# Optimization experiments

Hardware: AMD Instinct MI355X
Metric: run time of the kernel (lower is better)

The kernel has to match this reference:

```python
import jax, jax.numpy as jnp
import numpy as np

DIM = 192; HEADS = 6; WS = 7; RES = 56; SHIFT = 3
HEAD_DIM = DIM // HEADS
SCALE = HEAD_DIM ** -0.5
N = WS * WS
EPS = 1e-5

def _rel_pos_index():
    coords = np.stack(np.meshgrid(np.arange(WS), np.arange(WS), indexing='ij')).reshape(2, -1)
    rel = coords[:, :, None] - coords[:, None, :]  # [2,N,N]
    rel = rel.transpose(1, 2, 0)
    rel[:, :, 0] += WS - 1
    rel[:, :, 1] += WS - 1
    rel[:, :, 0] *= 2 * WS - 1
    return rel.sum(-1)  # [N,N]

def _attn_mask():
    img = np.zeros((RES, RES), dtype=np.float32)
    slices = (slice(0, -WS), slice(-WS, -SHIFT), slice(-SHIFT, None))
    cnt = 0
    for h in slices:
        for w in slices:
            img[h, w] = cnt; cnt += 1
    mw = img.reshape(RES // WS, WS, RES // WS, WS).transpose(0, 2, 1, 3).reshape(-1, N)  # [nW,N]
    diff = mw[:, None, :] - mw[:, :, None]
    return np.where(diff != 0, -100.0, 0.0).astype(np.float32)  # [nW,N,N]

REL_IDX = jnp.asarray(_rel_pos_index())
ATTN_MASK = jnp.asarray(_attn_mask())

def _ln(x, g, b):
    mu = x.mean(-1, keepdims=True)
    var = ((x - mu) ** 2).mean(-1, keepdims=True)
    return (x - mu) * jax.lax.rsqrt(var + EPS) * g + b

def setup_inputs() -> dict:
    key = jax.random.key(0)
    ks = jax.random.split(key, 8)
    d = {
        'x': jax.random.normal(ks[0], (32, RES * RES, DIM), jnp.float32),
        'norm1_g': jnp.ones((DIM,), jnp.float32), 'norm1_b': jnp.zeros((DIM,), jnp.float32),
        'qkv_w': jax.random.normal(ks[1], (DIM, 3 * DIM), jnp.float32) * 0.02,
        'qkv_b': jnp.zeros((3 * DIM,), jnp.float32),
        'proj_w': jax.random.normal(ks[2], (DIM, DIM), jnp.float32) * 0.02,
        'proj_b': jnp.zeros((DIM,), jnp.float32),
        'bias_table': jax.random.normal(ks[3], ((2 * WS - 1) ** 2, HEADS), jnp.float32) * 0.02,
        'norm2_g': jnp.ones((DIM,), jnp.float32), 'norm2_b': jnp.zeros((DIM,), jnp.float32),
        'fc1_w': jax.random.normal(ks[4], (DIM, 4 * DIM), jnp.float32) * 0.02,
        'fc1_b': jnp.zeros((4 * DIM,), jnp.float32),
        'fc2_w': jax.random.normal(ks[5], (4 * DIM, DIM), jnp.float32) * 0.02,
        'fc2_b': jnp.zeros((DIM,), jnp.float32),
    }
    return d

def reference(x, norm1_g, norm1_b, qkv_w, qkv_b, proj_w, proj_b, bias_table,
              norm2_g, norm2_b, fc1_w, fc1_b, fc2_w, fc2_b):
    B, L, C = x.shape
    H = W = RES
    shortcut = x
    h = _ln(x, norm1_g, norm1_b).reshape(B, H, W, C)
    # cyclic shift
    h = jnp.roll(h, (-SHIFT, -SHIFT), axis=(1, 2))
    # window partition -> [B*nW, N, C]
    nH = H // WS
    h = h.reshape(B, nH, WS, nH, WS, C).transpose(0, 1, 3, 2, 4, 5).reshape(-1, N, C)
    BW = h.shape[0]
    # windowed MHSA
    qkv = (h @ qkv_w + qkv_b).reshape(BW, N, 3, HEADS, HEAD_DIM)
    q, k, v = qkv[:, :, 0], qkv[:, :, 1], qkv[:, :, 2]  # [BW,N,h,hd]
    attn = jnp.einsum('bnhd,bmhd->bhnm', q, k) * SCALE  # [BW,h,N,N]
    bias = bias_table[REL_IDX.reshape(-1)].reshape(N, N, HEADS).transpose(2, 0, 1)
    attn = attn + bias[None]
    nW = ATTN_MASK.shape[0]
    attn = attn.reshape(BW // nW, nW, HEADS, N, N) + ATTN_MASK[None, :, None]
    attn = jax.nn.softmax(attn.reshape(BW, HEADS, N, N), axis=-1)
    h = jnp.einsum('bhnm,bmhd->bnhd', attn, v).reshape(BW, N, C)
    h = h @ proj_w + proj_b
    # window reverse
    h = h.reshape(B, nH, nH, WS, WS, C).transpose(0, 1, 3, 2, 4, 5).reshape(B, H, W, C)
    h = jnp.roll(h, (SHIFT, SHIFT), axis=(1, 2)).reshape(B, L, C)
    x = shortcut + h
    # MLP
    m = _ln(x, norm2_g, norm2_b)
    m = jax.nn.gelu(m @ fc1_w + fc1_b, approximate=False) @ fc2_w + fc2_b
    return x + m
```

## Files before the change

### kernel.cpp

```cpp
#include <hip/hip_runtime.h>
#include <hip/hip_bf16.h>
#include <math.h>

typedef __attribute__((ext_vector_type(8))) short bh8;
typedef __attribute__((ext_vector_type(4))) float fx4;

__device__ __forceinline__ fx4 mfma_bf16(bh8 a, bh8 b, fx4 c) {
    return __builtin_amdgcn_mfma_f32_16x16x32_bf16(a, b, c, 0, 0, 0);
}

__device__ __forceinline__ void gload16(const __hip_bfloat16* g, __hip_bfloat16* l) {
    __builtin_amdgcn_global_load_lds(
        (const __attribute__((address_space(1))) void*)g,
        (__attribute__((address_space(3))) void*)l,
        16, 0, 0);
}

__device__ __forceinline__ float fast_erf(float u) {
    float au = fabsf(u);
    float t  = __builtin_amdgcn_rcpf(1.0f + 0.3275911f * au);
    float p  = ((((1.061405429f * t - 1.453152027f) * t + 1.421413741f) * t
                 - 0.284496736f) * t + 0.254829592f) * t;
    float e  = __expf(-u * u);
    return copysignf(1.0f - p * e, u);
}

__global__ __launch_bounds__(256)
void convw_k(const float* __restrict__ W, __hip_bfloat16* __restrict__ Wt, int K, int Nn)
{
    int idx = blockIdx.x * 256 + threadIdx.x;
    if (idx < K * Nn) {
        int k = idx / Nn, n = idx - k * Nn;
        Wt[(size_t)n * K + k] = __float2bfloat16(W[idx]);
    }
}

__global__ __launch_bounds__(256)
void ln1_gather_k(const float* __restrict__ x, const float* __restrict__ g,
                  const float* __restrict__ bia, __hip_bfloat16* __restrict__ xw)
{
    const int wave = threadIdx.x >> 6, lane = threadIdx.x & 63;
    const int t = blockIdx.x * 4 + wave;
    const int w = t / 49, n = t - w * 49;
    const int b = w >> 6, wrem = w & 63, wi = wrem >> 3, wj = wrem & 7;
    const int i = n / 7, j = n - i * 7;
    int sr = wi * 7 + i + 3; if (sr >= 56) sr -= 56;
    int sc = wj * 7 + j + 3; if (sc >= 56) sc -= 56;
    const float* xp = x + ((size_t)b * 3136 + sr * 56 + sc) * 192;
    float v0 = xp[lane], v1 = xp[lane + 64], v2 = xp[lane + 128];
    float s = v0 + v1 + v2;
    float q = v0 * v0 + v1 * v1 + v2 * v2;
    for (int off = 32; off > 0; off >>= 1) {
        s += __shfl_down(s, off, 64);
        q += __shfl_down(q, off, 64);
    }
    s = __shfl(s, 0, 64); q = __shfl(q, 0, 64);
    float mean = s * (1.0f / 192.0f);
    float var  = q * (1.0f / 192.0f) - mean * mean;
    float rstd = rsqrtf(var + 1e-5f);
    __hip_bfloat16* op = xw + (size_t)t * 192;
    op[lane]       = __float2bfloat16((v0 - mean) * rstd * g[lane]       + bia[lane]);
    op[lane + 64]  = __float2bfloat16((v1 - mean) * rstd * g[lane + 64]  + bia[lane + 64]);
    op[lane + 128] = __float2bfloat16((v2 - mean) * rstd * g[lane + 128] + bia[lane + 128]);
}

template<int MODE, int K, int NOUT>
__global__ __launch_bounds__(256)
void gemm2_k(const __hip_bfloat16* __restrict__ A,
             const __hip_bfloat16* __restrict__ Bt,
             const float* __restrict__ bias,
             const float* __restrict__ resid,
             void* __restrict__ outv)
{
    __shared__ __align__(16) __hip_bfloat16 As[128 * 32];
    __shared__ __align__(16) __hip_bfloat16 Bs[64 * 32];
    const int tid  = threadIdx.x;
    const int lane = tid & 63, wave = tid >> 6;
    const int quad = lane >> 4, l15 = lane & 15;
    const int m0 = blockIdx.x * 128, n0 = blockIdx.y * 64;

    const int arow = lane >> 2, acol = (lane & 3) * 8;
    const __hip_bfloat16* Ag0 = A  + (size_t)(m0 + wave * 32 + arow)      * K + acol;
    const __hip_bfloat16* Ag1 = A  + (size_t)(m0 + wave * 32 + 16 + arow) * K + acol;
    const __hip_bfloat16* Bg  = Bt + (size_t)(n0 + wave * 16 + arow)      * K + acol;
    __hip_bfloat16* Al0 = &As[(wave * 32)      * 32];
    __hip_bfloat16* Al1 = &As[(wave * 32 + 16) * 32];
    __hip_bfloat16* Bl  = &Bs[(wave * 16)      * 32];

    fx4 acc[2][4];
#pragma unroll
    for (int mi = 0; mi < 2; mi++)
#pragma unroll
        for (int ni = 0; ni < 4; ni++) acc[mi][ni] = {0.f, 0.f, 0.f, 0.f};

    for (int k0 = 0; k0 < K; k0 += 32) {
        gload16(Ag0 + k0, Al0);
        gload16(Ag1 + k0, Al1);
        gload16(Bg  + k0, Bl);
        __syncthreads();
        bh8 a0 = *(const bh8*)&As[(wave * 32 + l15)      * 32 + quad * 8];
        bh8 a1 = *(const bh8*)&As[(wave * 32 + 16 + l15) * 32 + quad * 8];
        bh8 b0 = *(const bh8*)&Bs[(0 * 16 + l15) * 32 + quad * 8];
        bh8 b1 = *(const bh8*)&Bs[(1 * 16 + l15) * 32 + quad * 8];
        bh8 b2 = *(const bh8*)&Bs[(2 * 16 + l15) * 32 + quad * 8];
        bh8 b3 = *(const bh8*)&Bs[(3 * 16 + l15) * 32 + quad * 8];
        acc[0][0] = mfma_bf16(a0, b0, acc[0][0]);
        acc[0][1] = mfma_bf16(a0, b1, acc[0][1]);
        acc[0][2] = mfma_bf16(a0, b2, acc[0][2]);
        acc[0][3] = mfma_bf16(a0, b3, acc[0][3]);
        acc[1][0] = mfma_bf16(a1, b0, acc[1][0]);
        acc[1][1] = mfma_bf16(a1, b1, acc[1][1]);
        acc[1][2] = mfma_bf16(a1, b2, acc[1][2]);
        acc[1][3] = mfma_bf16(a1, b3, acc[1][3]);
        __syncthreads();
    }

#pragma unroll
    for (int mi = 0; mi < 2; mi++)
#pragma unroll
    for (int ni = 0; ni < 4; ni++) {
        const int n = n0 + ni * 16 + l15;
        const float bn = bias[n];
#pragma unroll
        for (int r = 0; r < 4; r++) {
            const int m = m0 + wave * 32 + mi * 16 + quad * 4 + r;
            float v = acc[mi][ni][r] + bn;
            if (MODE == 0) {
                if (n < 192) v *= 0.17677669529663687f;
                ((__hip_bfloat16*)outv)[(size_t)m * NOUT + n] = __float2bfloat16(v);
            } else if (MODE == 2) {
                v = 0.5f * v * (1.0f + erff(v * 0.70710678118654752f));
                ((__hip_bfloat16*)outv)[(size_t)m * NOUT + n] = __float2bfloat16(v);
            } else {
                ((float*)outv)[(size_t)m * NOUT + n] = v + resid[(size_t)m * NOUT + n];
            }
        }
    }
}

__global__ __launch_bounds__(256)
void mlp_k(const __hip_bfloat16* __restrict__ A,
           const __hip_bfloat16* __restrict__ W1t,
           const __hip_bfloat16* __restrict__ W2t,
           const float* __restrict__ b1,
           const float* __restrict__ b2,
           float* __restrict__ out)
{
    __shared__ __align__(16) __hip_bfloat16 W1s[2][6][32][32];
    __shared__ __align__(16) __hip_bfloat16 W2s[2][192][32];
    __shared__ __align__(16) __hip_bfloat16 Hs[64][40];

    const int tid  = threadIdx.x;
    const int lane = tid & 63, wave = tid >> 6;
    const int quad = lane >> 4, l15 = lane & 15;
    const int m0 = blockIdx.x * 64;
    const int arow = lane >> 2, acol = (lane & 3) * 8;

    bh8 xr[6];
    const __hip_bfloat16* xg = A + (size_t)(m0 + wave * 16 + l15) * 192 + quad * 8;
#pragma unroll
    for (int kc = 0; kc < 6; kc++) xr[kc] = *(const bh8*)(xg + kc * 32);

    auto stage = [&](int bf, int c) {
#pragma unroll
        for (int i = 0; i < 3; i++) {
            const int g = wave * 3 + i;
            const int kc = g >> 1, half = g & 1;
            gload16(W1t + (size_t)(c * 32 + half * 16 + arow) * 192 + kc * 32 + acol,
                    &W1s[bf][kc][half * 16][0]);
            gload16(W2t + (size_t)(g * 16 + arow) * 768 + c * 32 + acol,
                    &W2s[bf][g * 16][0]);
        }
    };

    fx4 acc2[12];
#pragma unroll
    for (int nt = 0; nt < 12; nt++) acc2[nt] = {0.f, 0.f, 0.f, 0.f};

    stage(0, 0);
    __syncthreads();

    int cur = 0;
    for (int c = 0; c < 24; c++) {
        if (c < 23) stage(cur ^ 1, c + 1);

        float b1v0 = b1[c * 32 + l15];
        float b1v1 = b1[c * 32 + 16 + l15];

        fx4 acc1[2];
        acc1[0] = {0.f, 0.f, 0.f, 0.f};
        acc1[1] = {0.f, 0.f, 0.f, 0.f};
#pragma unroll
        for (int kc = 0; kc < 6; kc++) {
#pragma unroll
            for (int ni = 0; ni < 2; ni++) {
                bh8 b = *(const bh8*)&W1s[cur][kc][ni * 16 + l15][quad * 8];
                acc1[ni] = mfma_bf16(xr[kc], b, acc1[ni]);
            }
        }

#pragma unroll
        for (int ni = 0; ni < 2; ni++) {
            const float bb = ni ? b1v1 : b1v0;
#pragma unroll
            for (int r = 0; r < 4; r++) {
                float v = acc1[ni][r] + bb;
                float h = 0.5f * v * (1.0f + fast_erf(v * 0.70710678118654752f));
                Hs[wave * 16 + quad * 4 + r][ni * 16 + l15] = __float2bfloat16(h);
            }
        }
        asm volatile("s_waitcnt lgkmcnt(0)" ::: "memory");
        __builtin_amdgcn_sched_barrier(0);

        bh8 ap = *(const bh8*)&Hs[wave * 16 + l15][quad * 8];
#pragma unroll
        for (int nt = 0; nt < 12; nt++) {
            bh8 b = *(const bh8*)&W2s[cur][nt * 16 + l15][quad * 8];
            acc2[nt] = mfma_bf16(ap, b, acc2[nt]);
        }

        __syncthreads();
        cur ^= 1;
    }

#pragma unroll
    for (int nt = 0; nt < 12; nt++) {
        const int n = nt * 16 + l15;
        const float bn = b2[n];
#pragma unroll
        for (int r = 0; r < 4; r++) {
            const int m = m0 + wave * 16 + quad * 4 + r;
            out[(size_t)m * 192 + n] += acc2[nt][r] + bn;
        }
    }
}

__global__ __launch_bounds__(256)
void projln_k(const __hip_bfloat16* __restrict__ A,
              const __hip_bfloat16* __restrict__ Bt,
              const float* __restrict__ pb,
              const float* __restrict__ xresid,
              const float* __restrict__ g2,
              const float* __restrict__ b2,
              float* __restrict__ x1out,
              __hip_bfloat16* __restrict__ y2out)
{
    __shared__ __align__(16) __hip_bfloat16 As[64 * 32];
    __shared__ __align__(16) __hip_bfloat16 Bs[192 * 32];
    const int tid  = threadIdx.x;
    const int lane = tid & 63, wave = tid >> 6;
    const int quad = lane >> 4, l15 = lane & 15;
    const int m0 = blockIdx.x * 64;

    const int arow = lane >> 2, acol = (lane & 3) * 8;
    const __hip_bfloat16* Ag = A + (size_t)(m0 + wave * 16 + arow) * 192 + acol;
    __hip_bfloat16* Al = &As[(wave * 16) * 32];
    const __hip_bfloat16* Bg0 = Bt + (size_t)((wave + 0) * 16 + arow) * 192 + acol;
    const __hip_bfloat16* Bg1 = Bt + (size_t)((wave + 4) * 16 + arow) * 192 + acol;
    const __hip_bfloat16* Bg2 = Bt + (size_t)((wave + 8) * 16 + arow) * 192 + acol;
    __hip_bfloat16* Bl0 = &Bs[((wave + 0) * 16) * 32];
    __hip_bfloat16* Bl1 = &Bs[((wave + 4) * 16) * 32];
    __hip_bfloat16* Bl2 = &Bs[((wave + 8) * 16) * 32];

    fx4 acc[12];
#pragma unroll
    for (int ct = 0; ct < 12; ct++) acc[ct] = {0.f, 0.f, 0.f, 0.f};

    for (int k0 = 0; k0 < 192; k0 += 32) {
        gload16(Ag  + k0, Al);
        gload16(Bg0 + k0, Bl0);
        gload16(Bg1 + k0, Bl1);
        gload16(Bg2 + k0, Bl2);
        __syncthreads();
        bh8 a = *(const bh8*)&As[(wave * 16 + l15) * 32 + quad * 8];
#pragma unroll
        for (int ct = 0; ct < 12; ct++) {
            bh8 b = *(const bh8*)&Bs[(ct * 16 + l15) * 32 + quad * 8];
            acc[ct] = mfma_bf16(a, b, acc[ct]);
        }
        __syncthreads();
    }

#pragma unroll
    for (int r = 0; r < 4; r++) {
        const int row = m0 + wave * 16 + quad * 4 + r;
        float vv[12];
        float s = 0.f, q = 0.f;
#pragma unroll
        for (int ct = 0; ct < 12; ct++) {
            const int col = ct * 16 + l15;
            float v = acc[ct][r] + pb[col] + xresid[(size_t)row * 192 + col];
            vv[ct] = v;
            x1out[(size_t)row * 192 + col] = v;
            s += v;
            q += v * v;
        }
        s += __shfl_xor(s, 1, 64);  q += __shfl_xor(q, 1, 64);
        s += __shfl_xor(s, 2, 64);  q += __shfl_xor(q, 2, 64);
        s += __shfl_xor(s, 4, 64);  q += __shfl_xor(q, 4, 64);
        s += __shfl_xor(s, 8, 64);  q += __shfl_xor(q, 8, 64);
        float mean = s * (1.0f / 192.0f);
        float var  = q * (1.0f / 192.0f) - mean * mean;
        float rstd = rsqrtf(var + 1e-5f);
#pragma unroll
        for (int ct = 0; ct < 12; ct++) {
            const int col = ct * 16 + l15;
            float y = (vv[ct] - mean) * rstd * g2[col] + b2[col];
            y2out[(size_t)row * 192 + col] = __float2bfloat16(y);
        }
    }
}

__global__ __launch_bounds__(256)
void attn_k(const __hip_bfloat16* __restrict__ qkv,
            const float* __restrict__ bias_table,
            __hip_bfloat16* __restrict__ aout)
{
    __shared__ __align__(16) __hip_bfloat16 Qb[64 * 32];
    __shared__ __align__(16) __hip_bfloat16 Kb[64 * 32];
    __shared__ __align__(16) __hip_bfloat16 Vt[32 * 64];
    __shared__ __align__(16) __hip_bfloat16 Ps[64 * 72];
    __shared__ float bias_h[169];

    const int tid  = threadIdx.x;
    const int lane = tid & 63, wave = tid >> 6;
    const int quad = lane >> 4, l15 = lane & 15;
    const int w = blockIdx.x / 6, hd = blockIdx.x % 6;
    const int b = w >> 6, wrem = w & 63, wi = wrem >> 3, wj = wrem & 7;
    const size_t base = (size_t)w * 49 * 576 + hd * 32;

    if (tid < 169) bias_h[tid] = bias_table[tid * 6 + hd];

    bh8 z = {0, 0, 0, 0, 0, 0, 0, 0};
    {
        int row = tid >> 2, ch = (tid & 3) * 8;
        if (row < 49) {
            *(bh8*)&Qb[row * 32 + ch] = *(const bh8*)(qkv + base + (size_t)row * 576 + ch);
            *(bh8*)&Kb[row * 32 + ch] = *(const bh8*)(qkv + base + (size_t)row * 576 + 192 + ch);
        } else {
            *(bh8*)&Qb[row * 32 + ch] = z;
            *(bh8*)&Kb[row * 32 + ch] = z;
        }
        *(bh8*)&Vt[tid * 8] = z;
    }
    __syncthreads();
    for (int idx = tid; idx < 49 * 32; idx += 256) {
        int n = idx >> 5, d = idx & 31;
        Vt[d * 64 + n] = qkv[base + (size_t)n * 576 + 384 + d];
    }
    __syncthreads();

    fx4 zf = {0.f, 0.f, 0.f, 0.f};
    bh8 aq = *(const bh8*)&Qb[(wave * 16 + l15) * 32 + quad * 8];
    fx4 sarr[4];
#pragma unroll
    for (int ni = 0; ni < 4; ni++) {
        bh8 bk = *(const bh8*)&Kb[(ni * 16 + l15) * 32 + quad * 8];
        sarr[ni] = mfma_bf16(aq, bk, zf);
    }

    int iarr[4], ria[4], cia[4], mbi[4];
#pragma unroll
    for (int r = 0; r < 4; r++) {
        int i = wave * 16 + quad * 4 + r;
        int ri = i / 7, ci = i - ri * 7;
        iarr[r] = i; ria[r] = ri; cia[r] = ci;
        int ar = wi * 7 + ri, ac = wj * 7 + ci;
        int br = (ar < 49) ? 0 : ((ar < 53) ? 1 : 2);
        int bc = (ac < 49) ? 0 : ((ac < 53) ? 1 : 2);
        mbi[r] = br * 3 + bc;
    }
    float vals[4][4];
#pragma unroll
    for (int ni = 0; ni < 4; ni++) {
        int jcol = ni * 16 + l15;
        int rj = jcol / 7, cj = jcol - rj * 7;
        int ar = wi * 7 + rj, ac = wj * 7 + cj;
        int br = (ar < 49) ? 0 : ((ar < 53) ? 1 : 2);
        int bc = (ac < 49) ? 0 : ((ac < 53) ? 1 : 2);
        int mbj = br * 3 + bc;
#pragma unroll
        for (int r = 0; r < 4; r++) {
            float v;
            if (jcol >= 49)            v = -1e30f;
            else if (iarr[r] >= 49)    v = 0.0f;
            else {
                int bidx = (ria[r] - rj + 6) * 13 + (cia[r] - cj + 6);
                v = sarr[ni][r] + bias_h[bidx] + ((mbi[r] != mbj) ? -100.0f : 0.0f);
            }
            vals[ni][r] = v;
        }
    }
#pragma unroll
    for (int r = 0; r < 4; r++) {
        float mx = fmaxf(fmaxf(vals[0][r], vals[1][r]), fmaxf(vals[2][r], vals[3][r]));
        mx = fmaxf(mx, __shfl_xor(mx, 1, 64));
        mx = fmaxf(mx, __shfl_xor(mx, 2, 64));
        mx = fmaxf(mx, __shfl_xor(mx, 4, 64));
        mx = fmaxf(mx, __shfl_xor(mx, 8, 64));
        float e0 = __expf(vals[0][r] - mx);
        float e1 = __expf(vals[1][r] - mx);
        float e2 = __expf(vals[2][r] - mx);
        float e3 = __expf(vals[3][r] - mx);
        float sm = e0 + e1 + e2 + e3;
        sm += __shfl_xor(sm, 1, 64);
        sm += __shfl_xor(sm, 2, 64);
        sm += __shfl_xor(sm, 4, 64);
        sm += __shfl_xor(sm, 8, 64);
        float inv = 1.0f / sm;
        int prow = (wave * 16 + quad * 4 + r) * 72;
        Ps[prow + 0 * 16 + l15] = __float2bfloat16(e0 * inv);
        Ps[prow + 1 * 16 + l15] = __float2bfloat16(e1 * inv);
        Ps[prow + 2 * 16 + l15] = __float2bfloat16(e2 * inv);
        Ps[prow + 3 * 16 + l15] = __float2bfloat16(e3 * inv);
    }
    __syncthreads();

    fx4 o0 = zf, o1 = zf;
#pragma unroll
    for (int k0 = 0; k0 < 64; k0 += 32) {
        bh8 ap  = *(const bh8*)&Ps[(wave * 16 + l15) * 72 + k0 + quad * 8];
        bh8 bv0 = *(const bh8*)&Vt[(l15)      * 64 + k0 + quad * 8];
        bh8 bv1 = *(const bh8*)&Vt[(16 + l15) * 64 + k0 + quad * 8];
        o0 = mfma_bf16(ap, bv0, o0);
        o1 = mfma_bf16(ap, bv1, o1);
    }

#pragma unroll
    for (int r = 0; r < 4; r++) {
        int m = wave * 16 + quad * 4 + r;
        if (m < 49) {
            int i = m / 7, j2 = m - i * 7;
            int orow = wi * 7 + i + 3;  if (orow >= 56) orow -= 56;
            int ocol = wj * 7 + j2 + 3; if (ocol >= 56) ocol -= 56;
            size_t t = (size_t)b * 3136 + orow * 56 + ocol;
            aout[t * 192 + hd * 32 + l15]      = __float2bfloat16(o0[r]);
            aout[t * 192 + hd * 32 + 16 + l15] = __float2bfloat16(o1[r]);
        }
    }
}

extern "C" void kernel_launch(void* const* d_in, const int* in_sizes, int n_in,
                              void* d_out, int out_size, void* d_ws, size_t ws_size,
                              hipStream_t stream)
{
    const float* x      = (const float*)d_in[0];
    const float* n1g    = (const float*)d_in[1];
    const float* n1b    = (const float*)d_in[2];
    const float* qkv_w  = (const float*)d_in[3];
    const float* qkv_b  = (const float*)d_in[4];
    const float* proj_w = (const float*)d_in[5];
    const float* proj_b = (const float*)d_in[6];
    const float* btab   = (const float*)d_in[7];
    const float* n2g    = (const float*)d_in[8];
    const float* n2b    = (const float*)d_in[9];
    const float* fc1_w  = (const float*)d_in[10];
    const float* fc1_b  = (const float*)d_in[11];
    const float* fc2_w  = (const float*)d_in[12];
    const float* fc2_b  = (const float*)d_in[13];

    char* ws = (char*)d_ws;
    __hip_bfloat16* buf1    = (__hip_bfloat16*)(ws + 0);
    __hip_bfloat16* buf2    = (__hip_bfloat16*)(ws + 38535168);
    __hip_bfloat16* wt_qkv  = (__hip_bfloat16*)(ws + 192675840);
    __hip_bfloat16* wt_proj = (__hip_bfloat16*)(ws + 192897024);
    __hip_bfloat16* wt_fc1  = (__hip_bfloat16*)(ws + 192970752);
    __hip_bfloat16* wt_fc2  = (__hip_bfloat16*)(ws + 193265664);
    float*          x1      = (float*)d_out;

    convw_k<<<dim3(432), 256, 0, stream>>>(qkv_w, wt_qkv, 192, 576);
    convw_k<<<dim3(144), 256, 0, stream>>>(proj_w, wt_proj, 192, 192);
    convw_k<<<dim3(576), 256, 0, stream>>>(fc1_w, wt_fc1, 192, 768);
    convw_k<<<dim3(576), 256, 0, stream>>>(fc2_w, wt_fc2, 768, 192);

    ln1_gather_k<<<dim3(25088), 256, 0, stream>>>(x, n1g, n1b, buf1);

    gemm2_k<0, 192, 576><<<dim3(784, 9), 256, 0, stream>>>(buf1, wt_qkv, qkv_b, nullptr, buf2);

    attn_k<<<dim3(12288), 256, 0, stream>>>(buf2, btab, buf1);

    projln_k<<<dim3(1568), 256, 0, stream>>>(buf1, wt_proj, proj_b, x, n2g, n2b, x1, buf1);

    mlp_k<<<dim3(1568), 256, 0, stream>>>(buf1, wt_fc1, wt_fc2, fc1_b, fc2_b, x1);
}
```

Measured before the change: 532.3 us.

## Deepen MLP weight prefetch to two stages with explicit vmcnt waits and priorities

Restructures the fused MLP kernel's loop to keep two chunks of W1/W2 loads in flight, using a counted vmcnt wait instead of a full __syncthreads drain. The b1 bias loads are prefetched two iterations ahead, and the last iteration is peeled. MFMA sections are wrapped in s_setprio to favour matrix issue. The aim is to hide global-to-LDS load latency behind compute. The cost is reliance on hand-counted vmcnt values, which must match the number of outstanding loads, or the kernel races.

New measurement: 536.0 us. About the same (+0.7%).

```diff
diff --git a/kernel.cpp b/kernel.cpp
--- a/kernel.cpp
+++ b/kernel.cpp
@@ -24,6 +24,15 @@
     float e  = __expf(-u * u);
     return copysignf(1.0f - p * e, u);
 }
+
+#define WAITV8 do { asm volatile("s_waitcnt vmcnt(8)" ::: "memory"); \
+                    __builtin_amdgcn_sched_barrier(0); } while (0)
+#define WAITV0 do { asm volatile("s_waitcnt vmcnt(0)" ::: "memory"); \
+                    __builtin_amdgcn_sched_barrier(0); } while (0)
+#define LGKM0  do { asm volatile("s_waitcnt lgkmcnt(0)" ::: "memory"); \
+                    __builtin_amdgcn_sched_barrier(0); } while (0)
+#define BARR   do { __builtin_amdgcn_s_barrier(); \
+                    __builtin_amdgcn_sched_barrier(0); } while (0)
 
 __global__ __launch_bounds__(256)
 void convw_k(const float* __restrict__ W, __hip_bfloat16* __restrict__ Wt, int K, int Nn)
@@ -178,18 +187,20 @@
     for (int nt = 0; nt < 12; nt++) acc2[nt] = {0.f, 0.f, 0.f, 0.f};
 
     stage(0, 0);
-    __syncthreads();
+    float b1a0 = b1[l15],      b1a1 = b1[16 + l15];
+    stage(1, 1);
+    float b1b0 = b1[32 + l15], b1b1 = b1[48 + l15];
+    float b1c0 = 0.f, b1c1 = 0.f;
 
     int cur = 0;
-    for (int c = 0; c < 24; c++) {
-        if (c < 23) stage(cur ^ 1, c + 1);
-
-        float b1v0 = b1[c * 32 + l15];
-        float b1v1 = b1[c * 32 + 16 + l15];
+    for (int c = 0; c < 23; ++c) {
+        WAITV8;
+        BARR;
 
         fx4 acc1[2];
         acc1[0] = {0.f, 0.f, 0.f, 0.f};
         acc1[1] = {0.f, 0.f, 0.f, 0.f};
+        __builtin_amdgcn_s_setprio(1);
 #pragma unroll
         for (int kc = 0; kc < 6; kc++) {
 #pragma unroll
@@ -198,10 +209,11 @@
                 acc1[ni] = mfma_bf16(xr[kc], b, acc1[ni]);
             }
         }
+        __builtin_amdgcn_s_setprio(0);
 
 #pragma unroll
         for (int ni = 0; ni < 2; ni++) {
-            const float bb = ni ? b1v1 : b1v0;
+            const float bb = ni ? b1a1 : b1a0;
 #pragma unroll
             for (int r = 0; r < 4; r++) {
                 float v = acc1[ni][r] + bb;
@@ -209,18 +221,59 @@
                 Hs[wave * 16 + quad * 4 + r][ni * 16 + l15] = __float2bfloat16(h);
             }
         }
-        asm volatile("s_waitcnt lgkmcnt(0)" ::: "memory");
-        __builtin_amdgcn_sched_barrier(0);
+        LGKM0;
 
         bh8 ap = *(const bh8*)&Hs[wave * 16 + l15][quad * 8];
+        __builtin_amdgcn_s_setprio(1);
 #pragma unroll
         for (int nt = 0; nt < 12; nt++) {
             bh8 b = *(const bh8*)&W2s[cur][nt * 16 + l15][quad * 8];
             acc2[nt] = mfma_bf16(ap, b, acc2[nt]);
         }
-
-        __syncthreads();
+        __builtin_amdgcn_s_setprio(0);
+
+        BARR;
+        if (c < 22) {
+            stage(cur, c + 2);
+            b1c0 = b1[(c + 2) * 32 + l15];
+            b1c1 = b1[(c + 2) * 32 + 16 + l15];
+        }
+        b1a0 = b1b0; b1a1 = b1b1;
+        b1b0 = b1c0; b1b1 = b1c1;
         cur ^= 1;
+    }
+
+    {
+        WAITV0;
+        BARR;
+        fx4 acc1[2];
+        acc1[0] = {0.f, 0.f, 0.f, 0.f};
+        acc1[1] = {0.f, 0.f, 0.f, 0.f};
+#pragma unroll
+        for (int kc = 0; kc < 6; kc++) {
+#pragma unroll
+            for (int ni = 0; ni < 2; ni++) {
+                bh8 b = *(const bh8*)&W1s[cur][kc][ni * 16 + l15][quad * 8];
+                acc1[ni] = mfma_bf16(xr[kc], b, acc1[ni]);
+            }
+        }
+#pragma unroll
+        for (int ni = 0; ni < 2; ni++) {
+            const float bb = ni ? b1a1 : b1a0;
+#pragma unroll
+            for (int r = 0; r < 4; r++) {
+                float v = acc1[ni][r] + bb;
+                float h = 0.5f * v * (1.0f + fast_erf(v * 0.70710678118654752f));
+                Hs[wave * 16 + quad * 4 + r][ni * 16 + l15] = __float2bfloat16(h);
+            }
+        }
+        LGKM0;
+        bh8 ap = *(const bh8*)&Hs[wave * 16 + l15][quad * 8];
+#pragma unroll
+        for (int nt = 0; nt < 12; nt++) {
+            bh8 b = *(const bh8*)&W2s[cur][nt * 16 + l15][quad * 8];
+            acc2[nt] = mfma_bf16(ap, b, acc2[nt]);
+        }
     }
 
 #pragma unroll
```

## Single-buffer MLP weight staging, swap MFMA operands, and cache fc1 bias in LDS

Applied to the files above, without the earlier changes.

The fused MLP kernel drops double-buffered LDS staging for W1/W2 and uses a single buffer with a sync before and after each chunk. It caps launch bounds at 4 blocks per CU to raise occupancy. It swaps the MFMA operand order so each lane holds four consecutive hidden columns, which lets the GELU output go to LDS as a packed 4-wide store. The fc1 bias is preloaded into LDS. Dropping the double buffer serializes weight loads with compute within a block, and relies on higher occupancy to hide that latency.

Result: faster. 514.2 us (-3.4%).

```diff
diff --git a/kernel.cpp b/kernel.cpp
--- a/kernel.cpp
+++ b/kernel.cpp
@@ -3,6 +3,7 @@
 #include <math.h>
 
 typedef __attribute__((ext_vector_type(8))) short bh8;
+typedef __attribute__((ext_vector_type(4))) short sh4;
 typedef __attribute__((ext_vector_type(4))) float fx4;
 
 __device__ __forceinline__ fx4 mfma_bf16(bh8 a, bh8 b, fx4 c) {
@@ -24,6 +25,9 @@
     float e  = __expf(-u * u);
     return copysignf(1.0f - p * e, u);
 }
+
+#define LGKM0  do { asm volatile("s_waitcnt lgkmcnt(0)" ::: "memory"); \
+                    __builtin_amdgcn_sched_barrier(0); } while (0)
 
 __global__ __launch_bounds__(256)
 void convw_k(const float* __restrict__ W, __hip_bfloat16* __restrict__ Wt, int K, int Nn)
@@ -138,7 +142,7 @@
     }
 }
 
-__global__ __launch_bounds__(256)
+__global__ __launch_bounds__(256, 4)
 void mlp_k(const __hip_bfloat16* __restrict__ A,
            const __hip_bfloat16* __restrict__ W1t,
            const __hip_bfloat16* __restrict__ W2t,
@@ -146,9 +150,10 @@
            const float* __restrict__ b2,
            float* __restrict__ out)
 {
-    __shared__ __align__(16) __hip_bfloat16 W1s[2][6][32][32];
-    __shared__ __align__(16) __hip_bfloat16 W2s[2][192][32];
+    __shared__ __align__(16) __hip_bfloat16 W1s[6][32][32];
+    __shared__ __align__(16) __hip_bfloat16 W2s[192][32];
     __shared__ __align__(16) __hip_bfloat16 Hs[64][40];
+    __shared__ __align__(16) float b1s[768];
 
     const int tid  = threadIdx.x;
     const int lane = tid & 63, wave = tid >> 6;
@@ -156,20 +161,26 @@
     const int m0 = blockIdx.x * 64;
     const int arow = lane >> 2, acol = (lane & 3) * 8;
 
+    if (tid < 192) ((fx4*)b1s)[tid] = ((const fx4*)b1)[tid];
+
     bh8 xr[6];
     const __hip_bfloat16* xg = A + (size_t)(m0 + wave * 16 + l15) * 192 + quad * 8;
 #pragma unroll
     for (int kc = 0; kc < 6; kc++) xr[kc] = *(const bh8*)(xg + kc * 32);
 
-    auto stage = [&](int bf, int c) {
-#pragma unroll
-        for (int i = 0; i < 3; i++) {
-            const int g = wave * 3 + i;
-            const int kc = g >> 1, half = g & 1;
-            gload16(W1t + (size_t)(c * 32 + half * 16 + arow) * 192 + kc * 32 + acol,
-                    &W1s[bf][kc][half * 16][0]);
-            gload16(W2t + (size_t)(g * 16 + arow) * 768 + c * 32 + acol,
-                    &W2s[bf][g * 16][0]);
+    auto stage = [&](int c) {
+#pragma unroll
+        for (int i = 0; i < 6; i++) {
+            const int g = wave * 6 + i;
+            if (g < 12) {
+                const int kc = g >> 1, half = g & 1;
+                gload16(W1t + (size_t)(c * 32 + half * 16 + arow) * 192 + kc * 32 + acol,
+                        &W1s[kc][half * 16][0]);
+            } else {
+                const int g2 = g - 12;
+                gload16(W2t + (size_t)(g2 * 16 + arow) * 768 + c * 32 + acol,
+                        &W2s[g2 * 16][0]);
+            }
         }
     };
 
@@ -177,15 +188,13 @@
 #pragma unroll
     for (int nt = 0; nt < 12; nt++) acc2[nt] = {0.f, 0.f, 0.f, 0.f};
 
-    stage(0, 0);
-    __syncthreads();
-
-    int cur = 0;
-    for (int c = 0; c < 24; c++) {
-        if (c < 23) stage(cur ^ 1, c + 1);
-
-        float b1v0 = b1[c * 32 + l15];
-        float b1v1 = b1[c * 32 + 16 + l15];
+    stage(0);
+
+    for (int c = 0; c < 24; ++c) {
+        __syncthreads();
+
+        fx4 bv0 = *(const fx4*)&b1s[c * 32 + quad * 4];
+        fx4 bv1 = *(const fx4*)&b1s[c * 32 + 16 + quad * 4];
 
         fx4 acc1[2];
         acc1[0] = {0.f, 0.f, 0.f, 0.f};
@@ -194,33 +203,36 @@
         for (int kc = 0; kc < 6; kc++) {
 #pragma unroll
             for (int ni = 0; ni < 2; ni++) {
-                bh8 b = *(const bh8*)&W1s[cur][kc][ni * 16 + l15][quad * 8];
-                acc1[ni] = mfma_bf16(xr[kc], b, acc1[ni]);
+                bh8 w = *(const bh8*)&W1s[kc][ni * 16 + l15][quad * 8];
+                acc1[ni] = mfma_bf16(w, xr[kc], acc1[ni]);
             }
         }
 
 #pragma unroll
         for (int ni = 0; ni < 2; ni++) {
-            const float bb = ni ? b1v1 : b1v0;
+            const fx4 bv = ni ? bv1 : bv0;
+            sh4 pk;
 #pragma unroll
             for (int r = 0; r < 4; r++) {
-                float v = acc1[ni][r] + bb;
+                float v = acc1[ni][r] + bv[r];
                 float h = 0.5f * v * (1.0f + fast_erf(v * 0.70710678118654752f));
-                Hs[wave * 16 + quad * 4 + r][ni * 16 + l15] = __float2bfloat16(h);
+                union { __hip_bfloat16 hb; short s; } u;
+                u.hb = __float2bfloat16(h);
+                pk[r] = u.s;
             }
-        }
-        asm volatile("s_waitcnt lgkmcnt(0)" ::: "memory");
-        __builtin_amdgcn_sched_barrier(0);
-
-        bh8 ap = *(const bh8*)&Hs[wave * 16 + l15][quad * 8];
+            *(sh4*)&Hs[wave * 16 + l15][ni * 16 + quad * 4] = pk;
+        }
+        LGKM0;
+
+        bh8 ha = *(const bh8*)&Hs[wave * 16 + l15][quad * 8];
 #pragma unroll
         for (int nt = 0; nt < 12; nt++) {
-            bh8 b = *(const bh8*)&W2s[cur][nt * 16 + l15][quad * 8];
-            acc2[nt] = mfma_bf16(ap, b, acc2[nt]);
-        }
-
-        __syncthreads();
-        cur ^= 1;
+            bh8 w2 = *(const bh8*)&W2s[nt * 16 + l15][quad * 8];
+            acc2[nt] = mfma_bf16(ha, w2, acc2[nt]);
+        }
+
+        __syncthreads();
+        if (c < 23) stage(c + 1);
     }
 
 #pragma unroll
```
